# Kernel tuning notes

Measured on AMD Instinct MI355X. Metric: run time of the kernel, lower is better.

## Reference

```python
import jax, jax.numpy as jnp
import numpy as np
from jax.scipy.special import ndtr, ndtri

B, N, K = 64, 4096, 128
MU, SIGMA = 0.0, 1.0
_TINY = 1e-7


def setup_inputs() -> dict:
    key = jax.random.key(0)
    k1, k2, k3 = jax.random.split(key, 3)
    C = jax.random.randint(k1, (B, N), 0, K)                      # labels [B,N]
    eps = jax.random.normal(k2, (B, N), dtype=jnp.float32)        # std-normal noise for upper bounds
    U = jax.random.uniform(k3, (B, N, K), dtype=jnp.float32)      # uniforms for inverse-CDF truncnorm
    return {
        "C": C,
        "eps": eps,
        "U": U,
        "mu": jnp.full((1,), MU, dtype=jnp.float32),
        "sigma": jnp.full((1,), SIGMA, dtype=jnp.float32),
    }


def reference(C, eps, U, mu, sigma):
    # Relabel ground-truth labels to 0..K-1 (torch.unique(..., return_inverse=True))
    _, C_new = jnp.unique(C, return_inverse=True)
    C_new = C_new.reshape(C.shape)                                # [B,N]
    Kdim = U.shape[-1]
    # upper bound per (b,i): u ~ N(mu, sigma), reparameterized
    u = mu.reshape(()) + sigma.reshape(()) * eps                  # [B,N]
    # truncnorm.rvs(-inf, u) via inverse CDF: z = Phi^{-1}(U * Phi(u))
    Uc = jnp.clip(U, _TINY, 1.0 - _TINY)
    Z = ndtri(Uc * ndtr(u)[..., None])                            # [B,N,K]
    # Z[b,i,C_new[b,i]] = u[b,i]
    onehot = C_new[..., None] == jnp.arange(Kdim)                 # [B,N,K] bool
    return jnp.where(onehot, u[..., None], Z)
```

## Files before the change

kernel.cpp:

```cpp
#include <hip/hip_runtime.h>
#include <math.h>


__global__ void presence_kernel(const int* __restrict__ C, int n,
                                unsigned* __restrict__ mask) {
    unsigned m0 = 0, m1 = 0, m2 = 0, m3 = 0;
    int stride = gridDim.x * blockDim.x;
    for (int i = blockIdx.x * blockDim.x + threadIdx.x; i < n; i += stride) {
        int c = C[i];
        unsigned bit = 1u << (c & 31);
        int w = (c >> 5) & 3;
        m0 |= (w == 0) ? bit : 0u;
        m1 |= (w == 1) ? bit : 0u;
        m2 |= (w == 2) ? bit : 0u;
        m3 |= (w == 3) ? bit : 0u;
    }
    #pragma unroll
    for (int off = 32; off > 0; off >>= 1) {
        m0 |= __shfl_down(m0, off, 64);
        m1 |= __shfl_down(m1, off, 64);
        m2 |= __shfl_down(m2, off, 64);
        m3 |= __shfl_down(m3, off, 64);
    }
    if ((threadIdx.x & 63) == 0) {
        if (m0) atomicOr(&mask[0], m0);
        if (m1) atomicOr(&mask[1], m1);
        if (m2) atomicOr(&mask[2], m2);
        if (m3) atomicOr(&mask[3], m3);
    }
}

__global__ void __launch_bounds__(256) map_kernel(
    const int* __restrict__ C,
    const float* __restrict__ eps,
    const float4* __restrict__ U4,
    const float* __restrict__ mu_p,
    const float* __restrict__ sigma_p,
    const unsigned* __restrict__ mask,
    float4* __restrict__ out4,
    int total4)
{
    int idx = blockIdx.x * blockDim.x + threadIdx.x;
    if (idx >= total4) return;
    int row = idx >> 5;
    int k0  = (idx & 31) << 2;

    float mu = mu_p[0];
    float sigma = sigma_p[0];
    float u = fmaf(sigma, eps[row], mu);
    float phi = 0.5f * erfcf(-u * 0.7071067811865476f);

    int c = C[row];
    unsigned w0 = mask[0], w1 = mask[1], w2 = mask[2], w3 = mask[3];
    int cw = c >> 5;
    unsigned below = (1u << (c & 31)) - 1u;
    int rank = __popc(w0 & ((0 < cw) ? 0xFFFFFFFFu : ((0 == cw) ? below : 0u)))
             + __popc(w1 & ((1 < cw) ? 0xFFFFFFFFu : ((1 == cw) ? below : 0u)))
             + __popc(w2 & ((2 < cw) ? 0xFFFFFFFFu : ((2 == cw) ? below : 0u)))
             + __popc(w3 & ((3 < cw) ? 0xFFFFFFFFu : ((3 == cw) ? below : 0u)));

    float4 Uv = U4[idx];
    const float lo = 1e-7f;
    const float hi = 0.99999988079071045f;
    float us0 = Uv.x, us1 = Uv.y, us2 = Uv.z, us3 = Uv.w;

    float p;
    p = fminf(fmaxf(us0, lo), hi) * phi;
    float z0 = -1.4142135623730951f * erfcinvf(2.0f * p);
    p = fminf(fmaxf(us1, lo), hi) * phi;
    float z1 = -1.4142135623730951f * erfcinvf(2.0f * p);
    p = fminf(fmaxf(us2, lo), hi) * phi;
    float z2 = -1.4142135623730951f * erfcinvf(2.0f * p);
    p = fminf(fmaxf(us3, lo), hi) * phi;
    float z3 = -1.4142135623730951f * erfcinvf(2.0f * p);

    float4 o;
    o.x = (k0 + 0 == rank) ? u : z0;
    o.y = (k0 + 1 == rank) ? u : z1;
    o.z = (k0 + 2 == rank) ? u : z2;
    o.w = (k0 + 3 == rank) ? u : z3;
    out4[idx] = o;
}

extern "C" void kernel_launch(void* const* d_in, const int* in_sizes, int n_in,
                              void* d_out, int out_size, void* d_ws, size_t ws_size,
                              hipStream_t stream) {
    const int*   C     = (const int*)d_in[0];
    const float* eps   = (const float*)d_in[1];
    const float4* U4   = (const float4*)d_in[2];
    const float* mu    = (const float*)d_in[3];
    const float* sigma = (const float*)d_in[4];
    float4* out4 = (float4*)d_out;
    unsigned* mask = (unsigned*)d_ws;

    int n = in_sizes[0];
    int total4 = out_size / 4;

    hipMemsetAsync(d_ws, 0, 4 * sizeof(unsigned), stream);
    presence_kernel<<<256, 256, 0, stream>>>(C, n, mask);

    int blocks = (total4 + 255) / 256;
    map_kernel<<<blocks, 256, 0, stream>>>(C, eps, U4, mu, sigma, mask, out4, total4);
}
```

Before: 287.2 us.

## Replace erfcinvf with Acklam ndtri approximation and precompute per-row u/phi

```diff
diff --git a/kernel.cpp b/kernel.cpp
--- a/kernel.cpp
+++ b/kernel.cpp
@@ -2,18 +2,72 @@
 #include <math.h>
 
 
-__global__ void presence_kernel(const int* __restrict__ C, int n,
-                                unsigned* __restrict__ mask) {
+__device__ __forceinline__ float ndtri_acklam(float p) {
+    const float omp = 1.0f - p;
+    const bool upper = p > 0.5f;
+    const float pm = upper ? omp : p;
+    float x;
+    if (pm < 0.02425f) {
+        float q = sqrtf(-2.0f * __logf(pm));
+        float num = -0.007784894002430293f;
+        num = fmaf(num, q, -0.3223964580411365f);
+        num = fmaf(num, q, -2.400758277161838f);
+        num = fmaf(num, q, -2.549732539343734f);
+        num = fmaf(num, q,  4.374664141464968f);
+        num = fmaf(num, q,  2.938163982698783f);
+        float den = 0.007784695709041462f;
+        den = fmaf(den, q, 0.3224671290700398f);
+        den = fmaf(den, q, 2.445134137142996f);
+        den = fmaf(den, q, 3.754408661907416f);
+        den = fmaf(den, q, 1.0f);
+        x = num * __builtin_amdgcn_rcpf(den);
+        if (upper) x = -x;
+    } else {
+        float q = p - 0.5f;
+        float r = q * q;
+        float num = -39.69683028665376f;
+        num = fmaf(num, r,  220.9460984245205f);
+        num = fmaf(num, r, -275.9285104469687f);
+        num = fmaf(num, r,  138.3577518672690f);
+        num = fmaf(num, r,  -30.66479806614716f);
+        num = fmaf(num, r,    2.506628277459239f);
+        float den = -54.47609879822406f;
+        den = fmaf(den, r,  161.5858368580409f);
+        den = fmaf(den, r, -155.6989798598866f);
+        den = fmaf(den, r,   66.80131188771972f);
+        den = fmaf(den, r,  -13.28068155288572f);
+        den = fmaf(den, r,    1.0f);
+        x = q * num * __builtin_amdgcn_rcpf(den);
+    }
+    return x;
+}
+
+__global__ void __launch_bounds__(256) row_kernel(
+    const int* __restrict__ C,
+    const float* __restrict__ eps,
+    const float* __restrict__ mu_p,
+    const float* __restrict__ sigma_p,
+    unsigned* __restrict__ mask,
+    float2* __restrict__ uphi,
+    int n)
+{
+    __shared__ unsigned sm[4];
+    if (threadIdx.x < 4) sm[threadIdx.x] = 0u;
+    __syncthreads();
+
+    int i = blockIdx.x * blockDim.x + threadIdx.x;
     unsigned m0 = 0, m1 = 0, m2 = 0, m3 = 0;
-    int stride = gridDim.x * blockDim.x;
-    for (int i = blockIdx.x * blockDim.x + threadIdx.x; i < n; i += stride) {
+    if (i < n) {
         int c = C[i];
+        float u = fmaf(sigma_p[0], eps[i], mu_p[0]);
+        float phi = 0.5f * erfcf(-u * 0.7071067811865476f);
+        uphi[i] = make_float2(u, phi);
         unsigned bit = 1u << (c & 31);
         int w = (c >> 5) & 3;
-        m0 |= (w == 0) ? bit : 0u;
-        m1 |= (w == 1) ? bit : 0u;
-        m2 |= (w == 2) ? bit : 0u;
-        m3 |= (w == 3) ? bit : 0u;
+        m0 = (w == 0) ? bit : 0u;
+        m1 = (w == 1) ? bit : 0u;
+        m2 = (w == 2) ? bit : 0u;
+        m3 = (w == 3) ? bit : 0u;
     }
     #pragma unroll
     for (int off = 32; off > 0; off >>= 1) {
@@ -23,19 +77,22 @@
         m3 |= __shfl_down(m3, off, 64);
     }
     if ((threadIdx.x & 63) == 0) {
-        if (m0) atomicOr(&mask[0], m0);
-        if (m1) atomicOr(&mask[1], m1);
-        if (m2) atomicOr(&mask[2], m2);
-        if (m3) atomicOr(&mask[3], m3);
+        if (m0) atomicOr(&sm[0], m0);
+        if (m1) atomicOr(&sm[1], m1);
+        if (m2) atomicOr(&sm[2], m2);
+        if (m3) atomicOr(&sm[3], m3);
+    }
+    __syncthreads();
+    if (threadIdx.x < 4) {
+        unsigned v = sm[threadIdx.x];
+        if (v) atomicOr(&mask[threadIdx.x], v);
     }
 }
 
 __global__ void __launch_bounds__(256) map_kernel(
     const int* __restrict__ C,
-    const float* __restrict__ eps,
     const float4* __restrict__ U4,
-    const float* __restrict__ mu_p,
-    const float* __restrict__ sigma_p,
+    const float2* __restrict__ uphi,
     const unsigned* __restrict__ mask,
     float4* __restrict__ out4,
     int total4)
@@ -45,10 +102,9 @@
     int row = idx >> 5;
     int k0  = (idx & 31) << 2;
 
-    float mu = mu_p[0];
-    float sigma = sigma_p[0];
-    float u = fmaf(sigma, eps[row], mu);
-    float phi = 0.5f * erfcf(-u * 0.7071067811865476f);
+    float2 up = uphi[row];
+    float u = up.x;
+    float phi = up.y;
 
     int c = C[row];
     unsigned w0 = mask[0], w1 = mask[1], w2 = mask[2], w3 = mask[3];
@@ -62,17 +118,16 @@
     float4 Uv = U4[idx];
     const float lo = 1e-7f;
     const float hi = 0.99999988079071045f;
-    float us0 = Uv.x, us1 = Uv.y, us2 = Uv.z, us3 = Uv.w;
 
-    float p;
-    p = fminf(fmaxf(us0, lo), hi) * phi;
-    float z0 = -1.4142135623730951f * erfcinvf(2.0f * p);
-    p = fminf(fmaxf(us1, lo), hi) * phi;
-    float z1 = -1.4142135623730951f * erfcinvf(2.0f * p);
-    p = fminf(fmaxf(us2, lo), hi) * phi;
-    float z2 = -1.4142135623730951f * erfcinvf(2.0f * p);
-    p = fminf(fmaxf(us3, lo), hi) * phi;
-    float z3 = -1.4142135623730951f * erfcinvf(2.0f * p);
+    float p0 = fminf(fmaxf(Uv.x, lo), hi) * phi;
+    float p1 = fminf(fmaxf(Uv.y, lo), hi) * phi;
+    float p2 = fminf(fmaxf(Uv.z, lo), hi) * phi;
+    float p3 = fminf(fmaxf(Uv.w, lo), hi) * phi;
+
+    float z0 = ndtri_acklam(p0);
+    float z1 = ndtri_acklam(p1);
+    float z2 = ndtri_acklam(p2);
+    float z3 = ndtri_acklam(p3);
 
     float4 o;
     o.x = (k0 + 0 == rank) ? u : z0;
@@ -91,14 +146,18 @@
     const float* mu    = (const float*)d_in[3];
     const float* sigma = (const float*)d_in[4];
     float4* out4 = (float4*)d_out;
+
     unsigned* mask = (unsigned*)d_ws;
+    float2* uphi = (float2*)((char*)d_ws + 256);
 
     int n = in_sizes[0];
     int total4 = out_size / 4;
 
     hipMemsetAsync(d_ws, 0, 4 * sizeof(unsigned), stream);
-    presence_kernel<<<256, 256, 0, stream>>>(C, n, mask);
 
-    int blocks = (total4 + 255) / 256;
-    map_kernel<<<blocks, 256, 0, stream>>>(C, eps, U4, mu, sigma, mask, out4, total4);
+    int rb = (n + 255) / 256;
+    row_kernel<<<rb, 256, 0, stream>>>(C, eps, mu, sigma, mask, uphi, n);
+
+    int mb = (total4 + 255) / 256;
+    map_kernel<<<mb, 256, 0, stream>>>(C, U4, uphi, mask, out4, total4);
 }
```

New measurement: 243.6 us. -15.2%, faster.
